# Performance work log

Hardware: AMD Instinct MI355X
Metric: run time of the kernel (lower is better)

Reference implementation:

```python
import jax, jax.numpy as jnp
import numpy as np

EMBED = 1024
HEADS = 16
HEAD_DIM = 64
FF = 4096
EPS = 1e-5


def _layernorm(x, g, b):
    mu = jnp.mean(x, axis=-1, keepdims=True)
    var = jnp.mean(jnp.square(x - mu), axis=-1, keepdims=True)
    return (x - mu) * jax.lax.rsqrt(var + EPS) * g + b


def setup_inputs() -> dict:
    key = jax.random.key(0)
    ks = jax.random.split(key, 12)
    s_in = 1.0 / np.sqrt(EMBED)
    s_hd = 1.0 / np.sqrt(HEADS * HEAD_DIM)
    s_ff = 1.0 / np.sqrt(FF)
    return {
        "x": jax.random.normal(ks[0], (4, 2048, EMBED), dtype=jnp.float32),
        "Wq": jax.random.uniform(ks[1], (HEADS, EMBED, HEAD_DIM), jnp.float32, -s_in, s_in),
        "Wk": jax.random.uniform(ks[2], (HEADS, EMBED, HEAD_DIM), jnp.float32, -s_in, s_in),
        "Wv": jax.random.uniform(ks[3], (HEADS, EMBED, HEAD_DIM), jnp.float32, -s_in, s_in),
        "Wo": jax.random.uniform(ks[4], (HEADS * HEAD_DIM, EMBED), jnp.float32, -s_hd, s_hd),
        "bo": jax.random.uniform(ks[5], (EMBED,), jnp.float32, -s_hd, s_hd),
        "W1": jax.random.uniform(ks[6], (EMBED, FF), jnp.float32, -s_in, s_in),
        "b1": jax.random.uniform(ks[7], (FF,), jnp.float32, -s_in, s_in),
        "W2": jax.random.uniform(ks[8], (FF, EMBED), jnp.float32, -s_ff, s_ff),
        "b2": jax.random.uniform(ks[9], (EMBED,), jnp.float32, -s_ff, s_ff),
        "ln1_g": jnp.ones((EMBED,), jnp.float32),
        "ln1_b": jnp.zeros((EMBED,), jnp.float32),
        "ln2_g": jnp.ones((EMBED,), jnp.float32),
        "ln2_b": jnp.zeros((EMBED,), jnp.float32),
    }


def reference(x, Wq, Wk, Wv, Wo, bo, W1, b1, W2, b2, ln1_g, ln1_b, ln2_g, ln2_b):
    B, T, C = x.shape
    h = _layernorm(x, ln1_g, ln1_b)
    # per-head projections, batched over heads: [B,H,T,Dh]
    q = jnp.einsum("btc,hcd->bhtd", h, Wq)
    k = jnp.einsum("btc,hcd->bhtd", h, Wk)
    v = jnp.einsum("btc,hcd->bhtd", h, Wv)
    scale = HEAD_DIM ** -0.5
    att = jnp.einsum("bhtd,bhsd->bhts", q, k) * scale  # [B,H,T,T]
    causal = jnp.tril(jnp.ones((T, T), dtype=bool))
    att = jnp.where(causal, att, -jnp.inf)
    att = jax.nn.softmax(att, axis=-1)
    out = jnp.einsum("bhts,bhsd->bhtd", att, v)  # [B,H,T,Dh]
    # concat heads (matches torch.cat over head outputs) -> [B,T,H*Dh]
    out = out.transpose(0, 2, 1, 3).reshape(B, T, HEADS * HEAD_DIM)
    x = x + out @ Wo + bo
    h2 = _layernorm(x, ln2_g, ln2_b)
    ff = jax.nn.relu(h2 @ W1 + b1) @ W2 + b2
    return x + ff
```

## Files before the change

### kernel.cpp

```cpp
#include <hip/hip_runtime.h>
#include <hip/hip_bf16.h>

#define EMBED 1024
#define HEADS 16
#define HEAD_DIM 64
#define FFDIM 4096
#define TSEQ 2048
#define BATCH 4
#define ROWS (BATCH * TSEQ)

typedef __bf16 bf16;
typedef __attribute__((ext_vector_type(8))) __bf16 bf16x8;
typedef __attribute__((ext_vector_type(4))) __bf16 bf16x4;
typedef __attribute__((ext_vector_type(4))) float f32x4;

typedef const __attribute__((address_space(1))) void* gvp;
typedef __attribute__((address_space(3))) void* svp;

__global__ __launch_bounds__(256) void conv_wqkv_t(
    const float* __restrict__ Wq, const float* __restrict__ Wk,
    const float* __restrict__ Wv, bf16* __restrict__ WqkvT) {
  __shared__ bf16 t[64][72];
  int tid = threadIdx.x;
  int k0 = blockIdx.x * 64;
  int head = blockIdx.y;
  int which = blockIdx.z;
  const float* src = which == 0 ? Wq : which == 1 ? Wk : Wv;
  float scale = which == 0 ? 0.125f * 1.44269504088896f : 1.0f;
  src += (size_t)head * 65536;
  bf16* dst = WqkvT + ((size_t)which * 1024 + head * 64) * 1024;
#pragma unroll
  for (int i = 0; i < 4; ++i) {
    int r = i * 16 + (tid >> 4);
    int c = (tid & 15) * 4;
    float4 v = *(const float4*)&src[(size_t)(k0 + r) * 64 + c];
    t[c + 0][r] = (bf16)(v.x * scale);
    t[c + 1][r] = (bf16)(v.y * scale);
    t[c + 2][r] = (bf16)(v.z * scale);
    t[c + 3][r] = (bf16)(v.w * scale);
  }
  __syncthreads();
#pragma unroll
  for (int i = 0; i < 2; ++i) {
    int r = i * 32 + (tid >> 3);
    int c = (tid & 7) * 8;
    bf16x8 o;
#pragma unroll
    for (int j = 0; j < 8; ++j) o[j] = t[r][c + j];
    *(bf16x8*)&dst[(size_t)r * 1024 + k0 + c] = o;
  }
}

__global__ __launch_bounds__(256) void transpose_conv(
    const float* __restrict__ W, bf16* __restrict__ WT, int K, int N) {
  __shared__ bf16 t[64][72];
  int tid = threadIdx.x;
  int n0 = blockIdx.x * 64, k0 = blockIdx.y * 64;
#pragma unroll
  for (int i = 0; i < 4; ++i) {
    int r = i * 16 + (tid >> 4);
    int c = (tid & 15) * 4;
    float4 v = *(const float4*)&W[(size_t)(k0 + r) * N + n0 + c];
    t[c + 0][r] = (bf16)v.x;
    t[c + 1][r] = (bf16)v.y;
    t[c + 2][r] = (bf16)v.z;
    t[c + 3][r] = (bf16)v.w;
  }
  __syncthreads();
#pragma unroll
  for (int i = 0; i < 2; ++i) {
    int r = i * 32 + (tid >> 3);
    int c = (tid & 7) * 8;
    bf16x8 o;
#pragma unroll
    for (int j = 0; j < 8; ++j) o[j] = t[r][c + j];
    *(bf16x8*)&WT[(size_t)(n0 + r) * K + k0 + c] = o;
  }
}

__global__ __launch_bounds__(256) void transpose_v(const bf16* __restrict__ v,
                                                   bf16* __restrict__ vt) {
  __shared__ bf16 t[64][72];
  int bh = blockIdx.y;
  int t0 = blockIdx.x * 64;
  const bf16* src = v + (size_t)bh * 131072;
  bf16* dst = vt + (size_t)bh * 131072;
  int tid = threadIdx.x;
#pragma unroll
  for (int i = 0; i < 2; ++i) {
    int c = tid + i * 256;
    int r = c >> 3, d0 = (c & 7) * 8;
    bf16x8 vv = *(const bf16x8*)&src[(size_t)(t0 + r) * 64 + d0];
#pragma unroll
    for (int j = 0; j < 8; ++j) t[d0 + j][r] = vv[j];
  }
  __syncthreads();
#pragma unroll
  for (int i = 0; i < 2; ++i) {
    int c = tid + i * 256;
    int r = c >> 3, s0 = (c & 7) * 8;
    bf16x8 o;
#pragma unroll
    for (int j = 0; j < 8; ++j) o[j] = t[r][s0 + j];
    *(bf16x8*)&dst[(size_t)r * 2048 + t0 + s0] = o;
  }
}

__global__ __launch_bounds__(256) void ln_kernel(
    const float* __restrict__ x, const float* __restrict__ g,
    const float* __restrict__ bta, bf16* __restrict__ out) {
  int row = blockIdx.x;
  const float* xr = x + (size_t)row * EMBED;
  float4 v = ((const float4*)xr)[threadIdx.x];
  float s1 = v.x + v.y + v.z + v.w;
  float s2 = v.x * v.x + v.y * v.y + v.z * v.z + v.w * v.w;
#pragma unroll
  for (int off = 1; off < 64; off <<= 1) {
    s1 += __shfl_xor(s1, off);
    s2 += __shfl_xor(s2, off);
  }
  __shared__ float red[8];
  int wid = threadIdx.x >> 6;
  int lane = threadIdx.x & 63;
  if (lane == 0) {
    red[wid * 2] = s1;
    red[wid * 2 + 1] = s2;
  }
  __syncthreads();
  s1 = red[0] + red[2] + red[4] + red[6];
  s2 = red[1] + red[3] + red[5] + red[7];
  float mu = s1 * (1.0f / EMBED);
  float var = s2 * (1.0f / EMBED) - mu * mu;
  float rs = rsqrtf(var + 1e-5f);
  float4 gv = ((const float4*)g)[threadIdx.x];
  float4 bv = ((const float4*)bta)[threadIdx.x];
  bf16x4 o;
  o[0] = (bf16)((v.x - mu) * rs * gv.x + bv.x);
  o[1] = (bf16)((v.y - mu) * rs * gv.y + bv.y);
  o[2] = (bf16)((v.z - mu) * rs * gv.z + bv.z);
  o[3] = (bf16)((v.w - mu) * rs * gv.w + bv.w);
  *(bf16x4*)(out + (size_t)row * EMBED + threadIdx.x * 4) = o;
}

template <int EPI>
__global__ __launch_bounds__(512, 1) void gemm256(
    const bf16* __restrict__ A, const bf16* __restrict__ BT,
    bf16* __restrict__ Cb, const float* __restrict__ bias, int M, int N,
    int K) {
  __shared__ __attribute__((aligned(16))) char lds[98304];
  int gx = gridDim.x;
  int nwg = gx * gridDim.y;
  int wgid = blockIdx.y * gx + blockIdx.x;
  int cpx = nwg >> 3;
  int swz = (wgid & 7) * cpx + (wgid >> 3);
  int m0 = (swz / gx) * 256, n0 = (swz % gx) * 256;
  int tid = threadIdx.x;
  int lane = tid & 63, wid = tid >> 6;
  int lr = lane & 15, lg = lane >> 4;
  int wrM = (wid >> 2) * 128;
  int wcN = (wid & 3) * 64;
  int crow = lane >> 2;
  int slotg = (lane & 3) ^ (crow & 3);
  int NT = K >> 5;
  size_t rb = (size_t)K * 2;

  auto stageA = [&](int t) {
    char* dst = lds + ((unsigned)t % 3u) * 32768u;
#pragma unroll
    for (int q = 0; q < 2; ++q) {
      int c = wid * 2 + q;
      const char* srcA = (const char*)A + (size_t)(m0 + c * 16 + crow) * rb +
                         (size_t)t * 64 + slotg * 16;
      __builtin_amdgcn_global_load_lds((gvp)srcA, (svp)(dst + c * 1024), 16, 0,
                                       0);
    }
  };
  auto stageB = [&](int t) {
    char* dst = lds + ((unsigned)t % 3u) * 32768u + 16384u;
#pragma unroll
    for (int q = 0; q < 2; ++q) {
      int c = wid * 2 + q;
      const char* srcB = (const char*)BT + (size_t)(n0 + c * 16 + crow) * rb +
                         (size_t)t * 64 + slotg * 16;
      __builtin_amdgcn_global_load_lds((gvp)srcB, (svp)(dst + c * 1024), 16, 0,
                                       0);
    }
  };

  stageA(0);
  stageB(0);
  stageA(1);
  stageB(1);
  f32x4 acc[8][4] = {};
  int swcol = ((lg ^ (lr & 3)) * 16);
  for (int t = 0; t < NT; ++t) {
    if (t == NT - 1)
      asm volatile("s_waitcnt vmcnt(0)" ::: "memory");
    else
      asm volatile("s_waitcnt vmcnt(4)" ::: "memory");
    __builtin_amdgcn_s_barrier();
    __builtin_amdgcn_sched_barrier(0);
    const char* Ab = lds + ((unsigned)t % 3u) * 32768u;
    const char* Bb = Ab + 16384;
    int tn = t + 2;
    bool st = tn < NT;
    bf16x8 bfr[4], afA[4], afB[4];
#pragma unroll
    for (int j = 0; j < 4; ++j)
      bfr[j] = *(const bf16x8*)(Bb + (wcN + j * 16 + lr) * 64 + swcol);
#pragma unroll
    for (int i = 0; i < 4; ++i)
      afA[i] = *(const bf16x8*)(Ab + (wrM + i * 16 + lr) * 64 + swcol);
    if (st) stageA(tn);
    __builtin_amdgcn_s_barrier();
    __builtin_amdgcn_sched_barrier(0);
    __builtin_amdgcn_s_setprio(1);
#pragma unroll
    for (int i = 0; i < 4; ++i)
#pragma unroll
      for (int j = 0; j < 4; ++j)
        acc[i][j] = __builtin_amdgcn_mfma_f32_16x16x32_bf16(afA[i], bfr[j],
                                                            acc[i][j], 0, 0, 0);
    __builtin_amdgcn_s_setprio(0);
    __builtin_amdgcn_sched_barrier(0);
#pragma unroll
    for (int i = 0; i < 4; ++i)
      afB[i] = *(const bf16x8*)(Ab + (wrM + 64 + i * 16 + lr) * 64 + swcol);
    if (st) stageB(tn);
    __builtin_amdgcn_s_barrier();
    __builtin_amdgcn_sched_barrier(0);
    __builtin_amdgcn_s_setprio(1);
#pragma unroll
    for (int i = 0; i < 4; ++i)
#pragma unroll
      for (int j = 0; j < 4; ++j)
        acc[4 + i][j] = __builtin_amdgcn_mfma_f32_16x16x32_bf16(
            afB[i], bfr[j], acc[4 + i][j], 0, 0, 0);
    __builtin_amdgcn_s_setprio(0);
    __builtin_amdgcn_sched_barrier(0);
  }
#pragma unroll
  for (int i = 0; i < 8; ++i) {
#pragma unroll
    for (int j = 0; j < 4; ++j) {
#pragma unroll
      for (int r = 0; r < 4; ++r) {
        int row = m0 + wrM + i * 16 + lg * 4 + r;
        int col = n0 + wcN + j * 16 + lr;
        float v = acc[i][j][r];
        if (EPI == 0) {
          int which = col >> 10, cc = col & 1023;
          int b = row >> 11, tt = row & 2047, h = cc >> 6, d = cc & 63;
          bf16* dst = Cb + (size_t)which * 8388608;
          dst[((size_t)((b << 4) + h) * TSEQ + tt) * HEAD_DIM + d] = (bf16)v;
        } else {
          size_t o = (size_t)row * N + col;
          float u = v + bias[col];
          Cb[o] = (bf16)(u > 0.f ? u : 0.f);
        }
      }
    }
  }
}

__global__ __launch_bounds__(512, 2) void gemm_res(
    const bf16* __restrict__ A, const bf16* __restrict__ BT,
    float* __restrict__ Cf, const float* __restrict__ bias,
    const float* __restrict__ resid, int M, int N, int K) {
  __shared__ __attribute__((aligned(16))) char lds[73728];
  int gx = gridDim.x;
  int nwg = gx * gridDim.y;
  int wgid = blockIdx.y * gx + blockIdx.x;
  int cpx = nwg >> 3;
  int swz = (wgid & 7) * cpx + (wgid >> 3);
  int m0 = (swz / gx) * 256, n0 = (swz % gx) * 128;
  int tid = threadIdx.x;
  int lane = tid & 63, wid = tid >> 6;
  int lr = lane & 15, lg = lane >> 4;
  int wrM = (wid >> 1) * 64;
  int wcN = (wid & 1) * 64;
  int crow = lane >> 2;
  int slotg = (lane & 3) ^ (crow & 3);
  int NT = K >> 5;
  size_t rb = (size_t)K * 2;

  auto stageA = [&](int t) {
    char* dst = lds + ((unsigned)t % 3u) * 24576u;
#pragma unroll
    for (int q = 0; q < 2; ++q) {
      int c = wid * 2 + q;
      const char* srcA = (const char*)A + (size_t)(m0 + c * 16 + crow) * rb +
                         (size_t)t * 64 + slotg * 16;
      __builtin_amdgcn_global_load_lds((gvp)srcA, (svp)(dst + c * 1024), 16, 0,
                                       0);
    }
  };
  auto stageB = [&](int t) {
    char* dst = lds + ((unsigned)t % 3u) * 24576u + 16384u;
    const char* srcB = (const char*)BT + (size_t)(n0 + wid * 16 + crow) * rb +
                       (size_t)t * 64 + slotg * 16;
    __builtin_amdgcn_global_load_lds((gvp)srcB, (svp)(dst + wid * 1024), 16, 0,
                                     0);
  };

  stageA(0);
  stageB(0);
  stageA(1);
  stageB(1);
  f32x4 acc[4][4] = {};
  int swcol = ((lg ^ (lr & 3)) * 16);
  for (int t = 0; t < NT; ++t) {
    if (t == NT - 1)
      asm volatile("s_waitcnt vmcnt(0)" ::: "memory");
    else
      asm volatile("s_waitcnt vmcnt(3)" ::: "memory");
    __builtin_amdgcn_s_barrier();
    __builtin_amdgcn_sched_barrier(0);
    const char* Ab = lds + ((unsigned)t % 3u) * 24576u;
    const char* Bb = Ab + 16384;
    int tn = t + 2;
    bool st = tn < NT;
    bf16x8 bfr[4], afA[2], afB[2];
#pragma unroll
    for (int j = 0; j < 4; ++j)
      bfr[j] = *(const bf16x8*)(Bb + (wcN + j * 16 + lr) * 64 + swcol);
#pragma unroll
    for (int i = 0; i < 2; ++i)
      afA[i] = *(const bf16x8*)(Ab + (wrM + i * 16 + lr) * 64 + swcol);
    if (st) stageA(tn);
    __builtin_amdgcn_s_barrier();
    __builtin_amdgcn_sched_barrier(0);
    __builtin_amdgcn_s_setprio(1);
#pragma unroll
    for (int i = 0; i < 2; ++i)
#pragma unroll
      for (int j = 0; j < 4; ++j)
        acc[i][j] = __builtin_amdgcn_mfma_f32_16x16x32_bf16(afA[i], bfr[j],
                                                            acc[i][j], 0, 0, 0);
    __builtin_amdgcn_s_setprio(0);
    __builtin_amdgcn_sched_barrier(0);
#pragma unroll
    for (int i = 0; i < 2; ++i)
      afB[i] = *(const bf16x8*)(Ab + (wrM + 32 + i * 16 + lr) * 64 + swcol);
    if (st) stageB(tn);
    __builtin_amdgcn_s_barrier();
    __builtin_amdgcn_sched_barrier(0);
    __builtin_amdgcn_s_setprio(1);
#pragma unroll
    for (int i = 0; i < 2; ++i)
#pragma unroll
      for (int j = 0; j < 4; ++j)
        acc[2 + i][j] = __builtin_amdgcn_mfma_f32_16x16x32_bf16(
            afB[i], bfr[j], acc[2 + i][j], 0, 0, 0);
    __builtin_amdgcn_s_setprio(0);
    __builtin_amdgcn_sched_barrier(0);
  }
#pragma unroll
  for (int i = 0; i < 4; ++i) {
#pragma unroll
    for (int j = 0; j < 4; ++j) {
#pragma unroll
      for (int r = 0; r < 4; ++r) {
        int row = m0 + wrM + i * 16 + lg * 4 + r;
        int col = n0 + wcN + j * 16 + lr;
        size_t o = (size_t)row * N + col;
        Cf[o] = resid[o] + bias[col] + acc[i][j][r];
      }
    }
  }
}

__global__ __launch_bounds__(256) void attn_kernel(
    const bf16* __restrict__ q, const bf16* __restrict__ k,
    const bf16* __restrict__ vt, bf16* __restrict__ out) {
  __shared__ __attribute__((aligned(16))) char ldsK[8192];
  __shared__ __attribute__((aligned(16))) char ldsV[8192];
  __shared__ __attribute__((aligned(16))) char ldsP[16384];
  int bh = blockIdx.x;
  int b = bh >> 4, h = bh & 15;
  const bf16* qb = q + (size_t)bh * TSEQ * HEAD_DIM;
  const bf16* kb = k + (size_t)bh * TSEQ * HEAD_DIM;
  const bf16* vb = vt + (size_t)bh * HEAD_DIM * TSEQ;
  int tid = threadIdx.x, lane = tid & 63, w = tid >> 6;
  int lr = lane & 15, lg = lane >> 4;
  int Q = 15 - blockIdx.y;
  int tw = Q * 128 + w * 32;
  int srow0 = tid >> 3;
  int scol = (tid & 7) * 16;
  bf16x8 aq[2][2];
#pragma unroll
  for (int rg = 0; rg < 2; ++rg)
#pragma unroll
    for (int kc = 0; kc < 2; ++kc)
      aq[rg][kc] = *(const bf16x8*)&qb[(size_t)(tw + rg * 16 + lr) * HEAD_DIM +
                                       kc * 32 + lg * 8];
  f32x4 o[2][4] = {};
  float sacc[2][4] = {};
  char* myP = ldsP + w * 4096;
  int nj = 2 * Q + 2;
  for (int j = 0; j < nj; ++j) {
#pragma unroll
    for (int i = 0; i < 2; ++i) {
      int rr = srow0 + i * 32;
      int sw = scol ^ ((rr & 7) << 4);
      *(bf16x8*)(ldsK + rr * 128 + sw) =
          *(const bf16x8*)&kb[(size_t)(j * 64 + rr) * HEAD_DIM + (scol >> 1)];
      *(bf16x8*)(ldsV + rr * 128 + sw) =
          *(const bf16x8*)&vb[(size_t)rr * TSEQ + j * 64 + (scol >> 1)];
    }
    __syncthreads();
    f32x4 s[2][4] = {};
#pragma unroll
    for (int nb = 0; nb < 4; ++nb) {
      int rowK = nb * 16 + lr;
#pragma unroll
      for (int kc = 0; kc < 2; ++kc) {
        int cb = (kc * 64 + lg * 16) ^ ((rowK & 7) << 4);
        bf16x8 bk = *(const bf16x8*)(ldsK + rowK * 128 + cb);
        s[0][nb] = __builtin_amdgcn_mfma_f32_16x16x32_bf16(aq[0][kc], bk,
                                                           s[0][nb], 0, 0, 0);
        s[1][nb] = __builtin_amdgcn_mfma_f32_16x16x32_bf16(aq[1][kc], bk,
                                                           s[1][nb], 0, 0, 0);
      }
    }
    if (j >= 2 * Q) {
#pragma unroll
      for (int rg = 0; rg < 2; ++rg)
#pragma unroll
        for (int nb = 0; nb < 4; ++nb)
#pragma unroll
          for (int r = 0; r < 4; ++r) {
            int sg = j * 64 + nb * 16 + lr;
            int tg = tw + rg * 16 + lg * 4 + r;
            if (sg > tg) s[rg][nb][r] = -1e30f;
          }
    }
#pragma unroll
    for (int rg = 0; rg < 2; ++rg) {
#pragma unroll
      for (int r = 0; r < 4; ++r) {
        int rowP = rg * 16 + lg * 4 + r;
        int swr = (rowP & 7) << 4;
        float psum = 0.f;
#pragma unroll
        for (int nb = 0; nb < 4; ++nb) {
          float p = exp2f(s[rg][nb][r] - 8.0f);
          psum += p;
          *(bf16*)(myP + rowP * 128 + (((nb * 16 + lr) * 2) ^ swr)) = (bf16)p;
        }
        sacc[rg][r] += psum;
      }
    }
#pragma unroll
    for (int kc = 0; kc < 2; ++kc) {
      int cb0 = (kc * 64 + lg * 16) ^ ((lr & 7) << 4);
      bf16x8 pa0 = *(const bf16x8*)(myP + lr * 128 + cb0);
      bf16x8 pa1 = *(const bf16x8*)(myP + (16 + lr) * 128 + cb0);
#pragma unroll
      for (int br = 0; br < 4; ++br) {
        int rowV = br * 16 + lr;
        int cbv = (kc * 64 + lg * 16) ^ ((rowV & 7) << 4);
        bf16x8 bv = *(const bf16x8*)(ldsV + rowV * 128 + cbv);
        o[0][br] =
            __builtin_amdgcn_mfma_f32_16x16x32_bf16(pa0, bv, o[0][br], 0, 0, 0);
        o[1][br] =
            __builtin_amdgcn_mfma_f32_16x16x32_bf16(pa1, bv, o[1][br], 0, 0, 0);
      }
    }
    __syncthreads();
  }
  float lrow[2][4];
#pragma unroll
  for (int rg = 0; rg < 2; ++rg)
#pragma unroll
    for (int r = 0; r < 4; ++r) {
      float su = sacc[rg][r];
#pragma unroll
      for (int off = 1; off < 16; off <<= 1) su += __shfl_xor(su, off);
      lrow[rg][r] = su;
    }
#pragma unroll
  for (int rg = 0; rg < 2; ++rg)
#pragma unroll
    for (int br = 0; br < 4; ++br)
#pragma unroll
      for (int r = 0; r < 4; ++r) {
        int t = tw + rg * 16 + lg * 4 + r;
        int d = br * 16 + lr;
        float val = o[rg][br][r] / lrow[rg][r];
        out[((size_t)(b * TSEQ) + t) * EMBED + h * HEAD_DIM + d] = (bf16)val;
      }
}

extern "C" void kernel_launch(void* const* d_in, const int* in_sizes, int n_in,
                              void* d_out, int out_size, void* d_ws,
                              size_t ws_size, hipStream_t stream) {
  const float* x = (const float*)d_in[0];
  const float* Wq = (const float*)d_in[1];
  const float* Wk = (const float*)d_in[2];
  const float* Wv = (const float*)d_in[3];
  const float* Wo = (const float*)d_in[4];
  const float* bo = (const float*)d_in[5];
  const float* W1 = (const float*)d_in[6];
  const float* b1 = (const float*)d_in[7];
  const float* W2 = (const float*)d_in[8];
  const float* b2 = (const float*)d_in[9];
  const float* g1 = (const float*)d_in[10];
  const float* be1 = (const float*)d_in[11];
  const float* g2 = (const float*)d_in[12];
  const float* be2 = (const float*)d_in[13];
  float* out = (float*)d_out;
  char* ws = (char*)d_ws;

  const size_t U = 16777216;
  bf16* h = (bf16*)(ws + 0 * U);
  bf16* qb = (bf16*)(ws + 1 * U);
  bf16* vtb = (bf16*)(ws + 0 * U);
  bf16* vnb = (bf16*)(ws + 3 * U);
  bf16* ao = (bf16*)(ws + 3 * U);
  float* x1 = (float*)(ws + 4 * U);
  bf16* h2 = (bf16*)(ws + 6 * U);
  bf16* ff1 = (bf16*)(ws + 0 * U);
  char* wbase = ws + 7 * U;
  bf16* WqkvT = (bf16*)(wbase);
  bf16* WoT = (bf16*)(wbase + 6291456);
  bf16* W1T = (bf16*)(wbase + 8388608);
  bf16* W2T = (bf16*)(wbase + 16777216);

  hipLaunchKernelGGL(conv_wqkv_t, dim3(16, 16, 3), dim3(256), 0, stream, Wq,
                     Wk, Wv, WqkvT);
  hipLaunchKernelGGL(transpose_conv, dim3(16, 16), dim3(256), 0, stream, Wo,
                     WoT, 1024, 1024);
  hipLaunchKernelGGL(transpose_conv, dim3(64, 16), dim3(256), 0, stream, W1,
                     W1T, 1024, 4096);
  hipLaunchKernelGGL(transpose_conv, dim3(16, 64), dim3(256), 0, stream, W2,
                     W2T, 4096, 1024);
  hipLaunchKernelGGL(ln_kernel, dim3(8192), dim3(256), 0, stream, x, g1, be1,
                     h);
  hipLaunchKernelGGL((gemm256<0>), dim3(12, 32), dim3(512), 0, stream, h,
                     WqkvT, qb, (const float*)nullptr, ROWS, 3072, 1024);
  hipLaunchKernelGGL(transpose_v, dim3(32, 64), dim3(256), 0, stream, vnb,
                     vtb);
  hipLaunchKernelGGL(attn_kernel, dim3(64, 16), dim3(256), 0, stream, qb,
                     qb + 8388608, vtb, ao);
  hipLaunchKernelGGL(gemm_res, dim3(8, 32), dim3(512), 0, stream, ao, WoT, x1,
                     bo, x, ROWS, 1024, 1024);
  hipLaunchKernelGGL(ln_kernel, dim3(8192), dim3(256), 0, stream, x1, g2, be2,
                     h2);
  hipLaunchKernelGGL((gemm256<3>), dim3(16, 32), dim3(512), 0, stream, h2, W1T,
                     ff1, b1, ROWS, 4096, 1024);
  hipLaunchKernelGGL(gemm_res, dim3(8, 32), dim3(512), 0, stream, ff1, W2T,
                     out, b2, x1, ROWS, 1024, 4096);
}
```

Measured before the change: 402.6 us.

## Switch attention to 32x32x16 MFMA and keep P in registers

Rewrites the attention inner loop to use 32x32x16 bf16 MFMAs with S computed transposed (K as A operand), so each lane holds one query row's scores. The softmax probabilities are packed to bf16 in registers and rearranged across half-waves with shuffles to form the PV MFMA operand, removing the LDS round trip for P and its shared buffer. Row sums become per-lane accumulators, which simplifies the final reduction. In exchange it adds cross-lane shuffles and depends on correct MFMA register-layout assumptions.

```diff
diff --git a/kernel.cpp b/kernel.cpp
--- a/kernel.cpp
+++ b/kernel.cpp
@@ -13,9 +13,17 @@
 typedef __attribute__((ext_vector_type(8))) __bf16 bf16x8;
 typedef __attribute__((ext_vector_type(4))) __bf16 bf16x4;
 typedef __attribute__((ext_vector_type(4))) float f32x4;
+typedef __attribute__((ext_vector_type(16))) float f32x16;
 
 typedef const __attribute__((address_space(1))) void* gvp;
 typedef __attribute__((address_space(3))) void* svp;
+
+__device__ inline unsigned pk2(float a, float b) {
+  union { bf16 h[2]; unsigned u; } x;
+  x.h[0] = (bf16)a;
+  x.h[1] = (bf16)b;
+  return x.u;
+}
 
 __global__ __launch_bounds__(256) void conv_wqkv_t(
     const float* __restrict__ Wq, const float* __restrict__ Wk,
@@ -375,28 +383,25 @@
     const bf16* __restrict__ vt, bf16* __restrict__ out) {
   __shared__ __attribute__((aligned(16))) char ldsK[8192];
   __shared__ __attribute__((aligned(16))) char ldsV[8192];
-  __shared__ __attribute__((aligned(16))) char ldsP[16384];
   int bh = blockIdx.x;
   int b = bh >> 4, h = bh & 15;
   const bf16* qb = q + (size_t)bh * TSEQ * HEAD_DIM;
   const bf16* kb = k + (size_t)bh * TSEQ * HEAD_DIM;
   const bf16* vb = vt + (size_t)bh * HEAD_DIM * TSEQ;
   int tid = threadIdx.x, lane = tid & 63, w = tid >> 6;
-  int lr = lane & 15, lg = lane >> 4;
+  int l31 = lane & 31, hi = lane >> 5;
   int Q = 15 - blockIdx.y;
   int tw = Q * 128 + w * 32;
+  int qrow = tw + l31;
   int srow0 = tid >> 3;
   int scol = (tid & 7) * 16;
-  bf16x8 aq[2][2];
-#pragma unroll
-  for (int rg = 0; rg < 2; ++rg)
-#pragma unroll
-    for (int kc = 0; kc < 2; ++kc)
-      aq[rg][kc] = *(const bf16x8*)&qb[(size_t)(tw + rg * 16 + lr) * HEAD_DIM +
-                                       kc * 32 + lg * 8];
-  f32x4 o[2][4] = {};
-  float sacc[2][4] = {};
-  char* myP = ldsP + w * 4096;
+  int swz31 = (l31 & 7) << 4;
+  bf16x8 aq[4];
+#pragma unroll
+  for (int f = 0; f < 4; ++f)
+    aq[f] = *(const bf16x8*)&qb[(size_t)qrow * HEAD_DIM + f * 16 + hi * 8];
+  f32x16 o0 = {}, o1 = {};
+  float sacc = 0.f;
   int nj = 2 * Q + 2;
   for (int j = 0; j < nj; ++j) {
 #pragma unroll
@@ -409,87 +414,66 @@
           *(const bf16x8*)&vb[(size_t)rr * TSEQ + j * 64 + (scol >> 1)];
     }
     __syncthreads();
-    f32x4 s[2][4] = {};
-#pragma unroll
-    for (int nb = 0; nb < 4; ++nb) {
-      int rowK = nb * 16 + lr;
-#pragma unroll
-      for (int kc = 0; kc < 2; ++kc) {
-        int cb = (kc * 64 + lg * 16) ^ ((rowK & 7) << 4);
-        bf16x8 bk = *(const bf16x8*)(ldsK + rowK * 128 + cb);
-        s[0][nb] = __builtin_amdgcn_mfma_f32_16x16x32_bf16(aq[0][kc], bk,
-                                                           s[0][nb], 0, 0, 0);
-        s[1][nb] = __builtin_amdgcn_mfma_f32_16x16x32_bf16(aq[1][kc], bk,
-                                                           s[1][nb], 0, 0, 0);
+    f32x16 s0 = {}, s1 = {};
+#pragma unroll
+    for (int f = 0; f < 4; ++f) {
+      int colb = (f * 32 + hi * 16) ^ swz31;
+      bf16x8 ka = *(const bf16x8*)(ldsK + l31 * 128 + colb);
+      bf16x8 kb2 = *(const bf16x8*)(ldsK + (32 + l31) * 128 + colb);
+      s0 = __builtin_amdgcn_mfma_f32_32x32x16_bf16(ka, aq[f], s0, 0, 0, 0);
+      s1 = __builtin_amdgcn_mfma_f32_32x32x16_bf16(kb2, aq[f], s1, 0, 0, 0);
+    }
+    if (j >= 2 * Q) {
+#pragma unroll
+      for (int reg = 0; reg < 16; ++reg) {
+        int key = j * 64 + (reg & 3) + 8 * (reg >> 2) + 4 * hi;
+        if (key > qrow) s0[reg] = -1e30f;
+        if (key + 32 > qrow) s1[reg] = -1e30f;
       }
     }
-    if (j >= 2 * Q) {
-#pragma unroll
-      for (int rg = 0; rg < 2; ++rg)
-#pragma unroll
-        for (int nb = 0; nb < 4; ++nb)
-#pragma unroll
-          for (int r = 0; r < 4; ++r) {
-            int sg = j * 64 + nb * 16 + lr;
-            int tg = tw + rg * 16 + lg * 4 + r;
-            if (sg > tg) s[rg][nb][r] = -1e30f;
-          }
-    }
-#pragma unroll
-    for (int rg = 0; rg < 2; ++rg) {
-#pragma unroll
-      for (int r = 0; r < 4; ++r) {
-        int rowP = rg * 16 + lg * 4 + r;
-        int swr = (rowP & 7) << 4;
-        float psum = 0.f;
-#pragma unroll
-        for (int nb = 0; nb < 4; ++nb) {
-          float p = exp2f(s[rg][nb][r] - 8.0f);
-          psum += p;
-          *(bf16*)(myP + rowP * 128 + (((nb * 16 + lr) * 2) ^ swr)) = (bf16)p;
-        }
-        sacc[rg][r] += psum;
-      }
-    }
-#pragma unroll
-    for (int kc = 0; kc < 2; ++kc) {
-      int cb0 = (kc * 64 + lg * 16) ^ ((lr & 7) << 4);
-      bf16x8 pa0 = *(const bf16x8*)(myP + lr * 128 + cb0);
-      bf16x8 pa1 = *(const bf16x8*)(myP + (16 + lr) * 128 + cb0);
-#pragma unroll
-      for (int br = 0; br < 4; ++br) {
-        int rowV = br * 16 + lr;
-        int cbv = (kc * 64 + lg * 16) ^ ((rowV & 7) << 4);
-        bf16x8 bv = *(const bf16x8*)(ldsV + rowV * 128 + cbv);
-        o[0][br] =
-            __builtin_amdgcn_mfma_f32_16x16x32_bf16(pa0, bv, o[0][br], 0, 0, 0);
-        o[1][br] =
-            __builtin_amdgcn_mfma_f32_16x16x32_bf16(pa1, bv, o[1][br], 0, 0, 0);
-      }
+    unsigned pk0[8], pk1[8];
+#pragma unroll
+    for (int p = 0; p < 8; ++p) {
+      float a0 = exp2f(s0[2 * p] - 8.f), b0 = exp2f(s0[2 * p + 1] - 8.f);
+      float a1 = exp2f(s1[2 * p] - 8.f), b1 = exp2f(s1[2 * p + 1] - 8.f);
+      sacc += (a0 + b0) + (a1 + b1);
+      pk0[p] = pk2(a0, b0);
+      pk1[p] = pk2(a1, b1);
+    }
+#pragma unroll
+    for (int ks = 0; ks < 4; ++ks) {
+      const unsigned* P = (ks >> 1) ? pk1 : pk0;
+      int kp = (ks & 1) * 4;
+      unsigned x0 = P[kp + 0], x1 = P[kp + 1];
+      unsigned x2 = P[kp + 2], x3 = P[kp + 3];
+      unsigned y0 = (unsigned)__shfl_xor((int)x0, 32);
+      unsigned y1 = (unsigned)__shfl_xor((int)x1, 32);
+      unsigned y2 = (unsigned)__shfl_xor((int)x2, 32);
+      unsigned y3 = (unsigned)__shfl_xor((int)x3, 32);
+      union { unsigned u[4]; bf16x8 v; } pa;
+      pa.u[0] = hi ? y2 : x0;
+      pa.u[1] = hi ? y3 : x1;
+      pa.u[2] = hi ? x2 : y0;
+      pa.u[3] = hi ? x3 : y1;
+      int colb = (ks * 32 + hi * 16) ^ swz31;
+      bf16x8 bv0 = *(const bf16x8*)(ldsV + l31 * 128 + colb);
+      bf16x8 bv1 = *(const bf16x8*)(ldsV + (32 + l31) * 128 + colb);
+      o0 = __builtin_amdgcn_mfma_f32_32x32x16_bf16(pa.v, bv0, o0, 0, 0, 0);
+      o1 = __builtin_amdgcn_mfma_f32_32x32x16_bf16(pa.v, bv1, o1, 0, 0, 0);
     }
     __syncthreads();
   }
-  float lrow[2][4];
-#pragma unroll
-  for (int rg = 0; rg < 2; ++rg)
-#pragma unroll
-    for (int r = 0; r < 4; ++r) {
-      float su = sacc[rg][r];
-#pragma unroll
-      for (int off = 1; off < 16; off <<= 1) su += __shfl_xor(su, off);
-      lrow[rg][r] = su;
-    }
-#pragma unroll
-  for (int rg = 0; rg < 2; ++rg)
-#pragma unroll
-    for (int br = 0; br < 4; ++br)
-#pragma unroll
-      for (int r = 0; r < 4; ++r) {
-        int t = tw + rg * 16 + lg * 4 + r;
-        int d = br * 16 + lr;
-        float val = o[rg][br][r] / lrow[rg][r];
-        out[((size_t)(b * TSEQ) + t) * EMBED + h * HEAD_DIM + d] = (bf16)val;
-      }
+  float tot = sacc + __shfl_xor(sacc, 32);
+#pragma unroll
+  for (int reg = 0; reg < 16; ++reg) {
+    int ql = (reg & 3) + 8 * (reg >> 2) + 4 * hi;
+    float lw = __shfl(tot, ql);
+    float rl = 1.0f / lw;
+    int t = tw + ql;
+    size_t o = ((size_t)(b * TSEQ) + t) * EMBED + h * HEAD_DIM;
+    out[o + l31] = (bf16)(o0[reg] * rl);
+    out[o + 32 + l31] = (bf16)(o1[reg] * rl);
+  }
 }
 
 extern "C" void kernel_launch(void* const* d_in, const int* in_sizes, int n_in,
```

After: 398.8 us. About the same (-1.0%).
